# Performance work log

Hardware: AMD Instinct MI355X
Metric: run time of the kernel (lower is better)

The kernel has to match this reference:

```python
import jax, jax.numpy as jnp
import numpy as np

B, N, C = 64, 196, 768
H = 12
HD = C // H            # 64
TOPK = int(0.25 * HD)  # 16
HIDDEN = int(C * 4.0)  # 3072
SCALE = HD ** -0.5
EPS = 1e-5


def layernorm(x, g, b):
    mu = jnp.mean(x, axis=-1, keepdims=True)
    var = jnp.var(x, axis=-1, keepdims=True)
    return (x - mu) * jax.lax.rsqrt(var + EPS) * g + b


def setup_inputs() -> dict:
    key = jax.random.key(0)
    ks = jax.random.split(key, 8)
    s = 0.02
    return {
        "x": jax.random.normal(ks[0], (B, N, C), jnp.float32),
        "norm1_g": jnp.ones((C,), jnp.float32),
        "norm1_b": jnp.zeros((C,), jnp.float32),
        "qk_w": jax.random.normal(ks[1], (2 * C, C), jnp.float32) * s,   # torch Linear [out,in], no bias
        "attn_proj_w": jax.random.normal(ks[2], (C, H * TOPK), jnp.float32) * s,
        "attn_proj_b": jnp.zeros((C,), jnp.float32),
        "norm2_g": jnp.ones((C,), jnp.float32),
        "norm2_b": jnp.zeros((C,), jnp.float32),
        "fc1_w": jax.random.normal(ks[3], (HIDDEN, C), jnp.float32) * s,
        "fc1_b": jnp.zeros((HIDDEN,), jnp.float32),
        "fc2_w": jax.random.normal(ks[4], (C, HIDDEN), jnp.float32) * s,
        "fc2_b": jnp.zeros((C,), jnp.float32),
    }


def reference(x, norm1_g, norm1_b, qk_w, attn_proj_w, attn_proj_b,
              norm2_g, norm2_b, fc1_w, fc1_b, fc2_w, fc2_b):
    # --- HomoAttention branch ---
    h = layernorm(x, norm1_g, norm1_b)                       # [B,N,C]
    qk = h @ qk_w.T                                          # [B,N,2C]
    qk = qk.reshape(B, N, 2, H, HD).transpose(2, 0, 3, 1, 4) # [2,B,H,N,HD]
    q, k = qk[0] * SCALE, qk[1]
    attn = jnp.einsum('bhnd,bhmd->bhnm', q, k)               # [B,H,N,N]
    top_vals, _ = jax.lax.top_k(attn, TOPK)                  # [B,H,N,TOPK]
    a = jax.nn.softmax(top_vals, axis=-1)
    a = a.transpose(0, 2, 1, 3).reshape(B, N, H * TOPK)      # [B,N,H*TOPK]
    x = x + a @ attn_proj_w.T + attn_proj_b

    # --- MLP branch ---
    h2 = layernorm(x, norm2_g, norm2_b)
    h2 = jax.nn.gelu(h2 @ fc1_w.T + fc1_b, approximate=False)
    x = x + h2 @ fc2_w.T + fc2_b
    return x
```

## Files before the change

kernel.cpp:

```cpp
#include <hip/hip_runtime.h>


#define BATCH 64
#define SEQ   196
#define CH    768
#define NHEAD 12
#define HDIM  64
#define TOPK  16
#define HID   3072
#define MROWS 12544
#define MHALF 6272
#define SCALE_F 0.125f
#define NEGBIG -3e38f

typedef __bf16 bf16x8 __attribute__((ext_vector_type(8)));
typedef float  f32x4  __attribute__((ext_vector_type(4)));

__device__ __forceinline__ unsigned short f2b(float f) {
    union { float f; unsigned int i; } c; c.f = f;
    unsigned int u = c.i;
    return (unsigned short)((u + 0x7fffu + ((u >> 16) & 1u)) >> 16);
}
__device__ __forceinline__ float b2f(unsigned short u) {
    union { unsigned int i; float f; } c; c.i = ((unsigned int)u) << 16; return c.f;
}

__device__ __forceinline__ float gelu_f(float v) {
    float u = v * (0.7978845608f + 0.0356774081f * v * v);
    float e = __expf(2.0f * u);
    float th = 1.0f - 2.0f / (e + 1.0f);
    return 0.5f * v * (1.0f + th);
}

__device__ __forceinline__ void async16(const unsigned short* g, unsigned short* l) {
    __builtin_amdgcn_global_load_lds(
        (const __attribute__((address_space(1))) unsigned int*)(g),
        (__attribute__((address_space(3))) unsigned int*)(l), 16, 0, 0);
}

__global__ __launch_bounds__(256) void f2b4_k(const float* __restrict__ s0, unsigned short* __restrict__ d0, int n0,
                                              const float* __restrict__ s1, unsigned short* __restrict__ d1, int n1,
                                              const float* __restrict__ s2, unsigned short* __restrict__ d2, int n2,
                                              const float* __restrict__ s3, unsigned short* __restrict__ d3, int n3)
{
    int idx = (blockIdx.x * 256 + threadIdx.x) * 4;
    const float* s; unsigned short* d; int n;
    if (idx < n0) { s = s0; d = d0; n = n0; }
    else {
        idx -= n0;
        if (idx < n1) { s = s1; d = d1; n = n1; }
        else {
            idx -= n1;
            if (idx < n2) { s = s2; d = d2; n = n2; }
            else { idx -= n2; s = s3; d = d3; n = n3; }
        }
    }
    if (idx < n) {
        float4 v = *(const float4*)(s + idx);
        ushort4 o;
        o.x = f2b(v.x); o.y = f2b(v.y); o.z = f2b(v.z); o.w = f2b(v.w);
        *(ushort4*)(d + idx) = o;
    }
}

template<bool INF32>
__global__ __launch_bounds__(256) void ln_k(const void* __restrict__ xin,
                                            const float* __restrict__ gw,
                                            const float* __restrict__ bw,
                                            unsigned short* __restrict__ out)
{
    const int row = blockIdx.x;
    const int tid = threadIdx.x;
    float v0, v1, v2;
    if constexpr (INF32) {
        const float* xr = (const float*)xin + (size_t)row * CH;
        v0 = xr[tid]; v1 = xr[tid + 256]; v2 = xr[tid + 512];
    } else {
        const unsigned short* xr = (const unsigned short*)xin + (size_t)row * CH;
        v0 = b2f(xr[tid]); v1 = b2f(xr[tid + 256]); v2 = b2f(xr[tid + 512]);
    }
    float s  = v0 + v1 + v2;
    float sq = v0*v0 + v1*v1 + v2*v2;
#pragma unroll
    for (int off = 32; off > 0; off >>= 1) {
        s  += __shfl_down(s, off, 64);
        sq += __shfl_down(sq, off, 64);
    }
    __shared__ __align__(16) float red[8];
    if ((tid & 63) == 0) { red[(tid >> 6) * 2] = s; red[(tid >> 6) * 2 + 1] = sq; }
    __syncthreads();
    s  = red[0] + red[2] + red[4] + red[6];
    sq = red[1] + red[3] + red[5] + red[7];
    float mu  = s * (1.0f / CH);
    float var = sq * (1.0f / CH) - mu * mu;
    float rs  = rsqrtf(var + 1e-5f);
    unsigned short* orow = out + (size_t)row * CH;
    orow[tid]       = f2b((v0 - mu) * rs * gw[tid]       + bw[tid]);
    orow[tid + 256] = f2b((v1 - mu) * rs * gw[tid + 256] + bw[tid + 256]);
    orow[tid + 512] = f2b((v2 - mu) * rs * gw[tid + 512] + bw[tid + 512]);
}

template<int TM, int TN, bool BIAS, int RES, bool GELU, bool OUTF>
__global__ __launch_bounds__(256, 4)
void gemm_bt(const unsigned short* __restrict__ A,
             const unsigned short* __restrict__ Bw,
             const float* __restrict__ bias,
             const void* __restrict__ resid,
             void* __restrict__ Cout,
             int M, int N, int K)
{
    constexpr int WROWS = (TM == 128) ? 2 : 1;
    constexpr int WCOLS = 4 / WROWS;
    constexpr int JF = TN / (16 * WCOLS);
    __shared__ __align__(16) unsigned short As[2][TM * 32];
    __shared__ __align__(16) unsigned short Bs[2][TN * 32];
    const int tid  = threadIdx.x;
    const int w    = tid >> 6;
    const int lane = tid & 63;

    const int gridN = gridDim.x, gridM = gridDim.y;
    const int lid = blockIdx.y * gridN + blockIdx.x;
    const int SG = 8 * gridN;
    const int sg = lid / SG, r = lid % SG;
    const int remM = gridM - sg * 8;
    int mloc, nloc;
    if (remM >= 8) { mloc = sg * 8 + (r & 7); nloc = r >> 3; }
    else           { mloc = sg * 8 + r % remM; nloc = r / remM; }
    const int tileM = mloc * TM;
    const int tileN = nloc * TN;

    const int wm = (w / WCOLS) * 64;
    const int wn = (w % WCOLS) * (JF * 16);
    const int q   = lane >> 4;
    const int l16 = lane & 15;
    const int csw = (q ^ (l16 & 3)) * 8;

    f32x4 acc[4][JF];
#pragma unroll
    for (int i = 0; i < 4; ++i)
#pragma unroll
        for (int j = 0; j < JF; ++j) acc[i][j] = (f32x4){0.f, 0.f, 0.f, 0.f};

    const int r0 = tid >> 2;
    const int g0 = ((tid & 3) ^ (r0 & 3)) * 8;

    const unsigned short* pB[TN / 64];
    const unsigned short* pA[TM / 64];
#pragma unroll
    for (int c = 0; c < TN / 64; ++c) pB[c] = Bw + (size_t)(tileN + r0 + c * 64) * K + g0;
#pragma unroll
    for (int c = 0; c < TM / 64; ++c) pA[c] = A + (size_t)(tileM + r0 + c * 64) * K + g0;

    auto stage = [&](int buf) {
#pragma unroll
        for (int c = 0; c < TN / 64; ++c) {
            async16(pB[c], &Bs[buf][(size_t)(c * 256 + w * 64) * 8]);
            pB[c] += 32;
        }
#pragma unroll
        for (int c = 0; c < TM / 64; ++c) {
            async16(pA[c], &As[buf][(size_t)(c * 256 + w * 64) * 8]);
            pA[c] += 32;
        }
    };

    const int kIters = K >> 5;
    stage(0);
    int cur = 0;
    for (int kt = 0; kt < kIters; ++kt) {
        __syncthreads();
        if (kt + 1 < kIters) stage(cur ^ 1);
        bf16x8 af[4], bfr[JF];
#pragma unroll
        for (int i = 0; i < 4; ++i)
            af[i] = *(const bf16x8*)&As[cur][(wm + i * 16 + l16) * 32 + csw];
#pragma unroll
        for (int j = 0; j < JF; ++j)
            bfr[j] = *(const bf16x8*)&Bs[cur][(wn + j * 16 + l16) * 32 + csw];
#pragma unroll
        for (int i = 0; i < 4; ++i)
#pragma unroll
            for (int j = 0; j < JF; ++j)
                acc[i][j] = __builtin_amdgcn_mfma_f32_16x16x32_bf16(af[i], bfr[j], acc[i][j], 0, 0, 0);
        cur ^= 1;
    }

#pragma unroll
    for (int i = 0; i < 4; ++i) {
#pragma unroll
        for (int r2 = 0; r2 < 4; ++r2) {
            int row = tileM + wm + i * 16 + q * 4 + r2;
#pragma unroll
            for (int j = 0; j < JF; ++j) {
                int col = tileN + wn + j * 16 + l16;
                float v = acc[i][j][r2];
                if (BIAS) v += bias[col];
                if (GELU) v = gelu_f(v);
                if (RES == 1) v += ((const float*)resid)[(size_t)row * N + col];
                if (RES == 2) v += b2f(((const unsigned short*)resid)[(size_t)row * N + col]);
                if (OUTF) ((float*)Cout)[(size_t)row * N + col] = v;
                else      ((unsigned short*)Cout)[(size_t)row * N + col] = f2b(v);
            }
        }
    }
}

template<int KC, bool BIAS, int RES, bool GELU, bool OUTF>
__global__ __launch_bounds__(512, 2)
void gemm8p(const unsigned short* __restrict__ A,
            const unsigned short* __restrict__ Bw,
            const float* __restrict__ bias,
            const void* __restrict__ resid,
            void* __restrict__ Cout,
            int M, int N)
{
    constexpr int T = KC / 64;
    __shared__ __align__(16) unsigned short As[2][256 * 64];
    __shared__ __align__(16) unsigned short Bs[2][256 * 64];
    const int tid  = threadIdx.x;
    const int w    = tid >> 6;
    const int lane = tid & 63;
    const int q    = lane >> 4;
    const int l16  = lane & 15;

    const int gridN = gridDim.x, gridM = gridDim.y;
    const int lid = blockIdx.y * gridN + blockIdx.x;
    const int SG = 8 * gridN;
    const int sg = lid / SG, rr = lid % SG;
    const int remM = gridM - sg * 8;
    int mloc, nloc;
    if (remM >= 8) { mloc = sg * 8 + (rr & 7); nloc = rr >> 3; }
    else           { mloc = sg * 8 + rr % remM; nloc = rr / remM; }
    const int tileM = mloc * 256, tileN = nloc * 256;

    const int wm = (w >> 2) * 128;
    const int wn = (w & 3) * 64;

    const int r0 = tid >> 3;
    const int g0 = (tid & 7) ^ (r0 & 7);
    const unsigned short* pA0 = A  + (size_t)(tileM + r0) * KC + g0 * 8;
    const unsigned short* pB0 = Bw + (size_t)(tileN + r0) * KC + g0 * 8;

    auto stageHT = [&](int v, int j) {
        const unsigned short* src = (j < 2 ? pA0 : pB0)
                                  + (size_t)(j & 1) * 128 * KC + (size_t)v * 64;
        unsigned short* dst = (j < 2 ? As[v & 1] : Bs[v & 1]) + (j & 1) * 8192 + w * 512;
        async16(src, dst);
        async16(src + (size_t)64 * KC, dst + 4096);
    };

    f32x4 acc[8][4];
#pragma unroll
    for (int i = 0; i < 8; ++i)
#pragma unroll
        for (int jn = 0; jn < 4; ++jn) acc[i][jn] = (f32x4){0.f, 0.f, 0.f, 0.f};

    stageHT(0, 0); stageHT(0, 1); stageHT(0, 2); stageHT(0, 3); stageHT(1, 0);
    asm volatile("s_waitcnt vmcnt(2)" ::: "memory");
    __builtin_amdgcn_s_barrier();

    const int arow = wm + l16;
    const int brow = wn + l16;
    const int xsw  = l16 & 7;

#pragma unroll 2
    for (int u = 0; u < T; ++u) {
        const unsigned short* Ab = As[u & 1];
        const unsigned short* Bb = Bs[u & 1];
        bf16x8 af[4][2], b0[2][2], b1[2][2];

#pragma unroll
        for (int m = 0; m < 4; ++m)
#pragma unroll
            for (int kk = 0; kk < 2; ++kk)
                af[m][kk] = *(const bf16x8*)&Ab[(arow + m * 16) * 64 + ((((kk << 2) | q) ^ xsw) << 3)];
#pragma unroll
        for (int n = 0; n < 2; ++n)
#pragma unroll
            for (int kk = 0; kk < 2; ++kk)
                b0[n][kk] = *(const bf16x8*)&Bb[(brow + n * 16) * 64 + ((((kk << 2) | q) ^ xsw) << 3)];
        if (u + 1 < T) stageHT(u + 1, 1);
        __builtin_amdgcn_s_barrier();
        asm volatile("s_waitcnt lgkmcnt(0)" ::: "memory");
        __builtin_amdgcn_sched_barrier(0);
        __builtin_amdgcn_s_setprio(1);
#pragma unroll
        for (int kk = 0; kk < 2; ++kk)
#pragma unroll
            for (int m = 0; m < 4; ++m)
#pragma unroll
                for (int n = 0; n < 2; ++n)
                    acc[m][n] = __builtin_amdgcn_mfma_f32_16x16x32_bf16(af[m][kk], b0[n][kk], acc[m][n], 0, 0, 0);
        __builtin_amdgcn_s_setprio(0);
        __builtin_amdgcn_s_barrier();

#pragma unroll
        for (int n = 0; n < 2; ++n)
#pragma unroll
            for (int kk = 0; kk < 2; ++kk)
                b1[n][kk] = *(const bf16x8*)&Bb[(brow + 32 + n * 16) * 64 + ((((kk << 2) | q) ^ xsw) << 3)];
        if (u + 1 < T) stageHT(u + 1, 2);
        __builtin_amdgcn_s_barrier();
        asm volatile("s_waitcnt lgkmcnt(0)" ::: "memory");
        __builtin_amdgcn_sched_barrier(0);
        __builtin_amdgcn_s_setprio(1);
#pragma unroll
        for (int kk = 0; kk < 2; ++kk)
#pragma unroll
            for (int m = 0; m < 4; ++m)
#pragma unroll
                for (int n = 0; n < 2; ++n)
                    acc[m][2 + n] = __builtin_amdgcn_mfma_f32_16x16x32_bf16(af[m][kk], b1[n][kk], acc[m][2 + n], 0, 0, 0);
        __builtin_amdgcn_s_setprio(0);
        __builtin_amdgcn_s_barrier();

#pragma unroll
        for (int m = 0; m < 4; ++m)
#pragma unroll
            for (int kk = 0; kk < 2; ++kk)
                af[m][kk] = *(const bf16x8*)&Ab[(arow + 64 + m * 16) * 64 + ((((kk << 2) | q) ^ xsw) << 3)];
        if (u + 1 < T) stageHT(u + 1, 3);
        __builtin_amdgcn_s_barrier();
        asm volatile("s_waitcnt lgkmcnt(0)" ::: "memory");
        __builtin_amdgcn_sched_barrier(0);
        __builtin_amdgcn_s_setprio(1);
#pragma unroll
        for (int kk = 0; kk < 2; ++kk)
#pragma unroll
            for (int m = 0; m < 4; ++m)
#pragma unroll
                for (int n = 0; n < 2; ++n)
                    acc[4 + m][2 + n] = __builtin_amdgcn_mfma_f32_16x16x32_bf16(af[m][kk], b1[n][kk], acc[4 + m][2 + n], 0, 0, 0);
        __builtin_amdgcn_s_setprio(0);
        __builtin_amdgcn_s_barrier();

        if (u + 2 < T) {
            stageHT(u + 2, 0);
            asm volatile("s_waitcnt vmcnt(2)" ::: "memory");
        } else if (u + 1 < T) {
            asm volatile("s_waitcnt vmcnt(0)" ::: "memory");
        }
        __builtin_amdgcn_s_barrier();
        __builtin_amdgcn_s_setprio(1);
#pragma unroll
        for (int kk = 0; kk < 2; ++kk)
#pragma unroll
            for (int m = 0; m < 4; ++m)
#pragma unroll
                for (int n = 0; n < 2; ++n)
                    acc[4 + m][n] = __builtin_amdgcn_mfma_f32_16x16x32_bf16(af[m][kk], b0[n][kk], acc[4 + m][n], 0, 0, 0);
        __builtin_amdgcn_s_setprio(0);
        __builtin_amdgcn_s_barrier();
    }

#pragma unroll
    for (int mh = 0; mh < 2; ++mh)
#pragma unroll
        for (int m = 0; m < 4; ++m)
#pragma unroll
            for (int r2 = 0; r2 < 4; ++r2) {
                const int row = tileM + wm + mh * 64 + m * 16 + q * 4 + r2;
#pragma unroll
                for (int nh = 0; nh < 2; ++nh)
#pragma unroll
                    for (int n = 0; n < 2; ++n) {
                        const int col = tileN + wn + nh * 32 + n * 16 + l16;
                        float v = acc[mh * 4 + m][nh * 2 + n][r2];
                        if (BIAS) v += bias[col];
                        if (GELU) v = gelu_f(v);
                        if (RES == 1) v += ((const float*)resid)[(size_t)row * N + col];
                        if (RES == 2) v += b2f(((const unsigned short*)resid)[(size_t)row * N + col]);
                        if (OUTF) ((float*)Cout)[(size_t)row * N + col] = v;
                        else      ((unsigned short*)Cout)[(size_t)row * N + col] = f2b(v);
                    }
            }
    (void)M;
}

__global__ __launch_bounds__(256) void attn_topk(const unsigned short* __restrict__ qk,
                                                 unsigned short* __restrict__ aout)
{
    const int bh = blockIdx.x;
    const int b = bh / NHEAD, h = bh % NHEAD;
    __shared__ __align__(16) unsigned short Qs[208 * 64];
    __shared__ __align__(16) unsigned short Ks[208 * 64];
    const int tid = threadIdx.x;

    for (int i = tid; i < 208 * 8; i += 256) {
        int row = i >> 3, c = i & 7;
        uint4 vq = make_uint4(0, 0, 0, 0), vk = vq;
        if (row < SEQ) {
            const uint4* gp = (const uint4*)(qk + ((size_t)(b * SEQ + row) * 1536 + h * 64));
            vq = gp[c];
            vk = gp[c + 96];
        }
        int slot = c ^ (row & 7);
        *(uint4*)&Qs[row * 64 + slot * 8] = vq;
        *(uint4*)&Ks[row * 64 + slot * 8] = vk;
    }
    __syncthreads();

    const int w = tid >> 6, lane = tid & 63;
    const int q = lane >> 4, l16 = lane & 15;

    for (int tn = w; tn < 13; tn += 4) {
        const int nrow = tn * 16 + l16;
        const int nsw = nrow & 7;
        bf16x8 bq0 = *(const bf16x8*)&Qs[nrow * 64 + ((0 * 4 + q) ^ nsw) * 8];
        bf16x8 bq1 = *(const bf16x8*)&Qs[nrow * 64 + ((1 * 4 + q) ^ nsw) * 8];

        float t[TOPK];
#pragma unroll
        for (int j = 0; j < TOPK; ++j) t[j] = NEGBIG;

        for (int tm = 0; tm < 12; ++tm) {
            const int mrow = tm * 16 + l16;
            const int msw = mrow & 7;
            bf16x8 ak0 = *(const bf16x8*)&Ks[mrow * 64 + ((0 * 4 + q) ^ msw) * 8];
            bf16x8 ak1 = *(const bf16x8*)&Ks[mrow * 64 + ((1 * 4 + q) ^ msw) * 8];
            f32x4 acc = (f32x4){0.f, 0.f, 0.f, 0.f};
            acc = __builtin_amdgcn_mfma_f32_16x16x32_bf16(ak0, bq0, acc, 0, 0, 0);
            acc = __builtin_amdgcn_mfma_f32_16x16x32_bf16(ak1, bq1, acc, 0, 0, 0);
#pragma unroll
            for (int r = 0; r < 4; ++r) {
                float v = acc[r];
#pragma unroll
                for (int j = 0; j < TOPK; ++j) {
                    float mx = fmaxf(t[j], v);
                    v = fminf(t[j], v);
                    t[j] = mx;
                }
            }
        }
        {
            const int mrow = 12 * 16 + l16;
            const int msw = mrow & 7;
            bf16x8 ak0 = *(const bf16x8*)&Ks[mrow * 64 + ((0 * 4 + q) ^ msw) * 8];
            bf16x8 ak1 = *(const bf16x8*)&Ks[mrow * 64 + ((1 * 4 + q) ^ msw) * 8];
            f32x4 acc = (f32x4){0.f, 0.f, 0.f, 0.f};
            acc = __builtin_amdgcn_mfma_f32_16x16x32_bf16(ak0, bq0, acc, 0, 0, 0);
            acc = __builtin_amdgcn_mfma_f32_16x16x32_bf16(ak1, bq1, acc, 0, 0, 0);
#pragma unroll
            for (int r = 0; r < 4; ++r) {
                float v = (q == 0) ? acc[r] : NEGBIG;
#pragma unroll
                for (int j = 0; j < TOPK; ++j) {
                    float mx = fmaxf(t[j], v);
                    v = fminf(t[j], v);
                    t[j] = mx;
                }
            }
        }

#pragma unroll
        for (int stage = 0; stage < 2; ++stage) {
            const int xm = 16 << stage;
            float bl[TOPK], c[TOPK];
#pragma unroll
            for (int j = 0; j < TOPK; ++j) bl[j] = __shfl_xor(t[j], xm, 64);
#pragma unroll
            for (int j = 0; j < TOPK; ++j) c[j] = fmaxf(t[j], bl[TOPK - 1 - j]);
#pragma unroll
            for (int s = 8; s >= 1; s >>= 1) {
#pragma unroll
                for (int i = 0; i < TOPK; ++i) {
                    if ((i & s) == 0) {
                        float mx = fmaxf(c[i], c[i + s]);
                        c[i + s] = fminf(c[i], c[i + s]);
                        c[i] = mx;
                    }
                }
            }
#pragma unroll
            for (int j = 0; j < TOPK; ++j) t[j] = c[j];
        }

        if (q == 0 && nrow < SEQ) {
            float e[TOPK], sum = 0.f;
#pragma unroll
            for (int j = 0; j < TOPK; ++j) { e[j] = __expf((t[j] - t[0]) * SCALE_F); sum += e[j]; }
            float inv = 1.0f / sum;
            unsigned int pk[8];
#pragma unroll
            for (int jj = 0; jj < 8; ++jj)
                pk[jj] = (unsigned int)f2b(e[2 * jj] * inv) |
                         ((unsigned int)f2b(e[2 * jj + 1] * inv) << 16);
            unsigned short* dst = aout + ((size_t)(b * SEQ + nrow)) * (NHEAD * TOPK) + h * TOPK;
            ((uint4*)dst)[0] = make_uint4(pk[0], pk[1], pk[2], pk[3]);
            ((uint4*)dst)[1] = make_uint4(pk[4], pk[5], pk[6], pk[7]);
        }
    }
}

extern "C" void kernel_launch(void* const* d_in, const int* in_sizes, int n_in,
                              void* d_out, int out_size, void* d_ws, size_t ws_size,
                              hipStream_t stream)
{
    const float* x    = (const float*)d_in[0];
    const float* g1   = (const float*)d_in[1];
    const float* bb1  = (const float*)d_in[2];
    const float* qkw  = (const float*)d_in[3];
    const float* pw   = (const float*)d_in[4];
    const float* pb   = (const float*)d_in[5];
    const float* g2   = (const float*)d_in[6];
    const float* bb2  = (const float*)d_in[7];
    const float* f1w  = (const float*)d_in[8];
    const float* f1b  = (const float*)d_in[9];
    const float* f2w  = (const float*)d_in[10];
    const float* f2bp = (const float*)d_in[11];
    float* out = (float*)d_out;

    char* ws = (char*)d_ws;
    const size_t SZ_H   = (size_t)MROWS * CH * 2;
    const size_t N_WQK  = (size_t)2 * CH * CH;
    const size_t N_WP   = (size_t)CH * (NHEAD * TOPK);
    const size_t N_WF   = (size_t)HID * CH;
    const size_t SZ_W   = (N_WQK + N_WP + 2 * N_WF) * 2;
    const size_t SZ_A   = (size_t)MROWS * (NHEAD * TOPK) * 2;
    const size_t SZ_QK  = (size_t)MROWS * 2 * CH * 2;
    const size_t SZ_GGF = (size_t)MROWS * HID * 2;

    unsigned short* hbuf = (unsigned short*)(ws);
    unsigned short* wqk  = (unsigned short*)(ws + SZ_H);
    unsigned short* wp   = wqk + N_WQK;
    unsigned short* wf1  = wp  + N_WP;
    unsigned short* wf2  = wf1 + N_WF;
    unsigned short* av   = (unsigned short*)(ws + SZ_H + SZ_W);
    unsigned short* qk   = (unsigned short*)(ws + SZ_H + SZ_W + SZ_A);
    unsigned short* gg   = qk;

    const size_t base = SZ_H + SZ_W + SZ_A;
    const bool fullMLP = ws_size >= base + SZ_GGF + SZ_H;
    const bool bx1     = fullMLP || ws_size >= base + SZ_QK + SZ_H;
    unsigned short* x1b = (unsigned short*)(ws + base + (fullMLP ? SZ_GGF : SZ_QK));
    float* x1 = out;

    {
        int total4 = (int)((N_WQK + N_WP + 2 * N_WF) / 4);
        f2b4_k<<<(total4 + 255) / 256, 256, 0, stream>>>(
            qkw, wqk, (int)N_WQK, pw, wp, (int)N_WP,
            f1w, wf1, (int)N_WF, f2w, wf2, (int)N_WF);
    }

    ln_k<true><<<MROWS, 256, 0, stream>>>(x, g1, bb1, hbuf);
    gemm8p<CH, false, 0, false, false><<<dim3(2 * CH / 256, MROWS / 256), 512, 0, stream>>>(
        hbuf, wqk, nullptr, nullptr, qk, MROWS, 2 * CH);
    attn_topk<<<BATCH * NHEAD, 256, 0, stream>>>(qk, av);

    if (bx1) {
        gemm_bt<64, 128, true, 1, false, false><<<dim3(6, 196), 256, 0, stream>>>(
            av, wp, pb, x, x1b, MROWS, CH, NHEAD * TOPK);
        ln_k<false><<<MROWS, 256, 0, stream>>>(x1b, g2, bb2, hbuf);
        if (fullMLP) {
            gemm8p<CH, true, 0, true, false><<<dim3(HID / 256, MROWS / 256), 512, 0, stream>>>(
                hbuf, wf1, f1b, nullptr, gg, MROWS, HID);
            gemm8p<HID, true, 2, false, true><<<dim3(CH / 256, MROWS / 256), 512, 0, stream>>>(
                gg, wf2, f2bp, x1b, out, MROWS, CH);
        } else {
            for (int half = 0; half < 2; ++half) {
                const size_t ro = (size_t)half * MHALF;
                gemm_bt<128, 128, true, 0, true, false><<<dim3(24, 49), 256, 0, stream>>>(
                    hbuf + ro * CH, wf1, f1b, nullptr, gg, MHALF, HID, CH);
                gemm_bt<64, 256, true, 2, false, true><<<dim3(3, 98), 256, 0, stream>>>(
                    gg, wf2, f2bp, x1b + ro * CH, out + ro * CH, MHALF, CH, HID);
            }
        }
    } else {
        gemm_bt<64, 128, true, 1, false, true><<<dim3(6, 196), 256, 0, stream>>>(
            av, wp, pb, x, x1, MROWS, CH, NHEAD * TOPK);
        ln_k<true><<<MROWS, 256, 0, stream>>>(x1, g2, bb2, hbuf);
        for (int half = 0; half < 2; ++half) {
            const size_t ro = (size_t)half * MHALF;
            gemm_bt<128, 128, true, 0, true, false><<<dim3(24, 49), 256, 0, stream>>>(
                hbuf + ro * CH, wf1, f1b, nullptr, gg, MHALF, HID, CH);
            gemm_bt<64, 256, true, 1, false, true><<<dim3(3, 98), 256, 0, stream>>>(
                gg, wf2, f2bp, x1 + ro * CH, out + ro * CH, MHALF, CH, HID);
        }
    }
}
```

Baseline: 448.6 us.

## Restructure GEMM prefetch into per-quadrant A/B stages with fewer barriers

Reorganizes async global-to-LDS staging in the 256x256 GEMM so A and B are loaded in row-quadrant chunks matching the order of the four MFMA phases, with B rows remapped so each chunk covers the rows the next phase reads. It drops per-phase lgkmcnt waits and several barriers, and uses vmcnt-based waits so only the chunk needed next must land. The aim is to cut synchronization stalls and overlap global loads with compute more tightly. Risk: subtle race conditions on the double-buffered LDS if the wait counts or remapped offsets are wrong.

```diff
diff --git a/kernel.cpp b/kernel.cpp
--- a/kernel.cpp
+++ b/kernel.cpp
@@ -238,16 +238,22 @@
 
     const int r0 = tid >> 3;
     const int g0 = (tid & 7) ^ (r0 & 7);
-    const unsigned short* pA0 = A  + (size_t)(tileM + r0) * KC + g0 * 8;
-    const unsigned short* pB0 = Bw + (size_t)(tileN + r0) * KC + g0 * 8;
-
-    auto stageHT = [&](int v, int j) {
-        const unsigned short* src = (j < 2 ? pA0 : pB0)
-                                  + (size_t)(j & 1) * 128 * KC + (size_t)v * 64;
-        unsigned short* dst = (j < 2 ? As[v & 1] : Bs[v & 1]) + (j & 1) * 8192 + w * 512;
-        async16(src, dst);
-        async16(src + (size_t)64 * KC, dst + 4096);
+    const int rB = r0 + (r0 & 32);
+    const unsigned short* pAsrc = A  + (size_t)(tileM + r0) * KC + g0 * 8;
+    const unsigned short* pBsrc = Bw + (size_t)(tileN + rB) * KC + g0 * 8;
+
+    auto stageA = [&](int v, int j) {
+        const unsigned short* s = pAsrc + (size_t)(j * 64) * KC + v * 64;
+        unsigned short* d = As[v & 1] + j * 4096 + w * 512;
+        async16(s, d);
+        async16(s + (size_t)128 * KC, d + 8192);
     };
+    auto stageB = [&](int v, int j) {
+        const unsigned short* s = pBsrc + (size_t)(j * 32) * KC + v * 64;
+        unsigned short* d = Bs[v & 1] + j * 2048 + (w * 8 + ((w & 4) << 3)) * 64;
+        async16(s, d);
+        async16(s + (size_t)128 * KC, d + 8192);
+    };
 
     f32x4 acc[8][4];
 #pragma unroll
@@ -255,9 +261,10 @@
 #pragma unroll
         for (int jn = 0; jn < 4; ++jn) acc[i][jn] = (f32x4){0.f, 0.f, 0.f, 0.f};
 
-    stageHT(0, 0); stageHT(0, 1); stageHT(0, 2); stageHT(0, 3); stageHT(1, 0);
-    asm volatile("s_waitcnt vmcnt(2)" ::: "memory");
+    stageA(0, 0); stageB(0, 0); stageB(0, 1); stageA(0, 1);
+    asm volatile("s_waitcnt vmcnt(4)" ::: "memory");
     __builtin_amdgcn_s_barrier();
+    asm volatile("" ::: "memory");
 
     const int arow = wm + l16;
     const int brow = wn + l16;
@@ -279,10 +286,7 @@
 #pragma unroll
             for (int kk = 0; kk < 2; ++kk)
                 b0[n][kk] = *(const bf16x8*)&Bb[(brow + n * 16) * 64 + ((((kk << 2) | q) ^ xsw) << 3)];
-        if (u + 1 < T) stageHT(u + 1, 1);
-        __builtin_amdgcn_s_barrier();
-        asm volatile("s_waitcnt lgkmcnt(0)" ::: "memory");
-        __builtin_amdgcn_sched_barrier(0);
+        if (u + 1 < T) stageA(u + 1, 0);
         __builtin_amdgcn_s_setprio(1);
 #pragma unroll
         for (int kk = 0; kk < 2; ++kk)
@@ -292,17 +296,17 @@
                 for (int n = 0; n < 2; ++n)
                     acc[m][n] = __builtin_amdgcn_mfma_f32_16x16x32_bf16(af[m][kk], b0[n][kk], acc[m][n], 0, 0, 0);
         __builtin_amdgcn_s_setprio(0);
+
+        if (u + 1 < T) asm volatile("s_waitcnt vmcnt(4)" ::: "memory");
+        else           asm volatile("s_waitcnt vmcnt(2)" ::: "memory");
         __builtin_amdgcn_s_barrier();
-
+        asm volatile("" ::: "memory");
 #pragma unroll
         for (int n = 0; n < 2; ++n)
 #pragma unroll
             for (int kk = 0; kk < 2; ++kk)
                 b1[n][kk] = *(const bf16x8*)&Bb[(brow + 32 + n * 16) * 64 + ((((kk << 2) | q) ^ xsw) << 3)];
-        if (u + 1 < T) stageHT(u + 1, 2);
-        __builtin_amdgcn_s_barrier();
-        asm volatile("s_waitcnt lgkmcnt(0)" ::: "memory");
-        __builtin_amdgcn_sched_barrier(0);
+        if (u + 1 < T) stageB(u + 1, 0);
         __builtin_amdgcn_s_setprio(1);
 #pragma unroll
         for (int kk = 0; kk < 2; ++kk)
@@ -312,17 +316,17 @@
                 for (int n = 0; n < 2; ++n)
                     acc[m][2 + n] = __builtin_amdgcn_mfma_f32_16x16x32_bf16(af[m][kk], b1[n][kk], acc[m][2 + n], 0, 0, 0);
         __builtin_amdgcn_s_setprio(0);
+
+        if (u + 1 < T) asm volatile("s_waitcnt vmcnt(4)" ::: "memory");
+        else           asm volatile("s_waitcnt vmcnt(0)" ::: "memory");
         __builtin_amdgcn_s_barrier();
-
+        asm volatile("" ::: "memory");
 #pragma unroll
         for (int m = 0; m < 4; ++m)
 #pragma unroll
             for (int kk = 0; kk < 2; ++kk)
                 af[m][kk] = *(const bf16x8*)&Ab[(arow + 64 + m * 16) * 64 + ((((kk << 2) | q) ^ xsw) << 3)];
-        if (u + 1 < T) stageHT(u + 1, 3);
-        __builtin_amdgcn_s_barrier();
-        asm volatile("s_waitcnt lgkmcnt(0)" ::: "memory");
-        __builtin_amdgcn_sched_barrier(0);
+        if (u + 1 < T) stageB(u + 1, 1);
         __builtin_amdgcn_s_setprio(1);
 #pragma unroll
         for (int kk = 0; kk < 2; ++kk)
@@ -332,15 +336,13 @@
                 for (int n = 0; n < 2; ++n)
                     acc[4 + m][2 + n] = __builtin_amdgcn_mfma_f32_16x16x32_bf16(af[m][kk], b1[n][kk], acc[4 + m][2 + n], 0, 0, 0);
         __builtin_amdgcn_s_setprio(0);
-        __builtin_amdgcn_s_barrier();
-
-        if (u + 2 < T) {
-            stageHT(u + 2, 0);
-            asm volatile("s_waitcnt vmcnt(2)" ::: "memory");
-        } else if (u + 1 < T) {
-            asm volatile("s_waitcnt vmcnt(0)" ::: "memory");
-        }
-        __builtin_amdgcn_s_barrier();
+
+        if (u + 1 < T) {
+            stageA(u + 1, 1);
+            asm volatile("s_waitcnt vmcnt(4)" ::: "memory");
+            __builtin_amdgcn_s_barrier();
+            asm volatile("" ::: "memory");
+        }
         __builtin_amdgcn_s_setprio(1);
 #pragma unroll
         for (int kk = 0; kk < 2; ++kk)
@@ -350,7 +352,6 @@
                 for (int n = 0; n < 2; ++n)
                     acc[4 + m][n] = __builtin_amdgcn_mfma_f32_16x16x32_bf16(af[m][kk], b0[n][kk], acc[4 + m][n], 0, 0, 0);
         __builtin_amdgcn_s_setprio(0);
-        __builtin_amdgcn_s_barrier();
     }
 
 #pragma unroll
```

Result: faster. 436.8 us (-2.6%).
